# Optimization experiments

Hardware: AMD Instinct MI355X
Metric: run time of the kernel (lower is better)

Reference implementation:

```python
import jax, jax.numpy as jnp
import numpy as np

K = 64            # number of keypoints
PATCH = 16        # patch size
NUM_CLASSES = 1000
K_HARRIS = 0.04


def _conv3x3(x, w):
    # x: [N, Cin, H, W], w: [Cout, Cin, 3, 3], stride 1, padding 1 (torch conv2d = cross-correlation)
    return jax.lax.conv_general_dilated(x, w, (1, 1), 'SAME',
                                        dimension_numbers=('NCHW', 'OIHW', 'NCHW'))


def _harris_coords(x, k, patch_size):
    B, C, H, W = x.shape
    g = jnp.mean(x, axis=1, keepdims=True) if C != 1 else x  # grayscale [B,1,H,W]
    dxk = jnp.array([[-1., 0., 1.], [-1., 0., 1.], [-1., 0., 1.]], x.dtype).reshape(1, 1, 3, 3)
    dyk = jnp.array([[-1., -1., -1.], [0., 0., 0.], [1., 1., 1.]], x.dtype).reshape(1, 1, 3, 3)
    gauss = (jnp.array([[1., 2., 1.], [2., 4., 2.], [1., 2., 1.]], x.dtype) / 16.0).reshape(1, 1, 3, 3)
    dx = _conv3x3(g, dxk)
    dy = _conv3x3(g, dyk)
    Sxx = _conv3x3(dx * dx, gauss)
    Syy = _conv3x3(dy * dy, gauss)
    Sxy = _conv3x3(dx * dy, gauss)
    R = Sxx * Syy - Sxy ** 2 - K_HARRIS * (Sxx + Syy) ** 2  # [B,1,H,W]
    m = patch_size
    mask = jnp.zeros((H, W), x.dtype).at[m:H - m, m:W - m].set(1.0)
    R_flat = (R[:, 0] * mask).reshape(B, -1)
    _, idx = jax.lax.top_k(R_flat, k)                        # [B,k]
    coords = jnp.stack([idx // W, idx % W], axis=-1).astype(jnp.float32)  # (row, col)
    coords = (coords / jnp.array([H, W], jnp.float32) - 0.5) * 2.0
    return jnp.clip(coords, -1.0, 1.0)                       # [B,k,2]


def _grid_sample_bilinear(img, grid):
    # img: [N,C,H,W]; grid: [N,Hg,Wg,2] with (x, y) in [-1,1]; align_corners=True, zeros padding
    N, C, H, W = img.shape
    Hg, Wg = grid.shape[1], grid.shape[2]
    gx = (grid[..., 0] + 1.0) * 0.5 * (W - 1)
    gy = (grid[..., 1] + 1.0) * 0.5 * (H - 1)
    x0 = jnp.floor(gx); y0 = jnp.floor(gy)
    x1 = x0 + 1.0;      y1 = y0 + 1.0
    wx1 = gx - x0; wx0 = 1.0 - wx1
    wy1 = gy - y0; wy0 = 1.0 - wy1

    img_flat = img.reshape(N, C, H * W)

    def gather(xi, yi):
        valid = ((xi >= 0) & (xi < W) & (yi >= 0) & (yi < H)).astype(img.dtype)
        xc = jnp.clip(xi, 0, W - 1).astype(jnp.int32)
        yc = jnp.clip(yi, 0, H - 1).astype(jnp.int32)
        flat = (yc * W + xc).reshape(N, 1, Hg * Wg)
        vals = jnp.take_along_axis(img_flat, flat, axis=2).reshape(N, C, Hg, Wg)
        return vals * valid[:, None]

    out = (gather(x0, y0) * (wx0 * wy0)[:, None]
           + gather(x1, y0) * (wx1 * wy0)[:, None]
           + gather(x0, y1) * (wx0 * wy1)[:, None]
           + gather(x1, y1) * (wx1 * wy1)[:, None])
    return out


def _extract_patches(images, keypoints, patch_size):
    B, C, H, W = images.shape
    k = keypoints.shape[1]
    coords01 = (keypoints + 1.0) / 2.0                       # [B,k,2] (y,x) in [0,1]
    r = patch_size / H
    pg = jnp.linspace(-r, r, patch_size)
    yy, xx = jnp.meshgrid(pg, pg, indexing='ij')
    base = jnp.stack([xx, yy], axis=-1)[None, None]          # [1,1,P,P,2] (x_off, y_off)
    grid = base + coords01[:, :, None, None, :]              # faithful to original broadcast
    grid = grid * 2.0 - 1.0
    grid = grid.reshape(B * k, patch_size, patch_size, 2)
    x_exp = jnp.repeat(images, k, axis=0)                    # repeat_interleave on batch
    patches = _grid_sample_bilinear(x_exp, grid)             # [B*k,C,P,P]
    return patches.reshape(B, k, C, patch_size, patch_size)


def _classify(patches, conv_w, conv_b, fc1_w, fc1_b, fc2_w, fc2_b):
    B, k, C, H, W = patches.shape
    p = patches.reshape(B * k, C, H, W)
    h = _conv3x3(p, conv_w) + conv_b[None, :, None, None]
    h = jax.nn.relu(h)
    h = h.reshape(B * k, -1)                                 # [B*k, 8*P*P]
    h = jax.nn.relu(h @ fc1_w.T + fc1_b)                     # [B*k, 64]
    h = h.reshape(B, k * 64)
    return h @ fc2_w.T + fc2_b                               # [B, num_classes]


def setup_inputs() -> dict:
    key = jax.random.key(0)
    ks = jax.random.split(key, 7)
    B, C, H, W = 32, 3, 224, 224
    return {
        'x': jax.random.normal(ks[0], (B, C, H, W), dtype=jnp.float32),
        'conv_w': jax.random.normal(ks[1], (8, C, 3, 3), dtype=jnp.float32) * 0.1,
        'conv_b': jax.random.normal(ks[2], (8,), dtype=jnp.float32) * 0.05,
        'fc1_w': jax.random.normal(ks[3], (64, 8 * PATCH * PATCH), dtype=jnp.float32) * 0.02,
        'fc1_b': jax.random.normal(ks[4], (64,), dtype=jnp.float32) * 0.05,
        'fc2_w': jax.random.normal(ks[5], (NUM_CLASSES, 64 * K), dtype=jnp.float32) * 0.02,
        'fc2_b': jax.random.normal(ks[6], (NUM_CLASSES,), dtype=jnp.float32) * 0.05,
    }


def reference(x, conv_w, conv_b, fc1_w, fc1_b, fc2_w, fc2_b):
    coords = _harris_coords(x, K, PATCH)                     # [B,K,2]
    patches = _extract_patches(x, coords, PATCH)             # [B,K,C,P,P]
    return _classify(patches, conv_w, conv_b, fc1_w, fc1_b, fc2_w, fc2_b)
```

## Files before the change

### kernel.cpp

```cpp
#include <hip/hip_runtime.h>
#include <cstdint>
#include <math.h>

#define HW 224
#define NPIX (HW*HW)
#define BATCH 32
#define KP 64
#define PS 16
#define NCLS 1000
#define TKW 112
#define FC1_KS 16

__device__ __forceinline__ uint64_t tk_pack(float v, int idx) {
    uint32_t u = __float_as_uint(v);
    u = (u & 0x80000000u) ? ~u : (u | 0x80000000u);
    return ((uint64_t)u << 32) | (uint32_t)(~idx);
}

__device__ __forceinline__ uint64_t tk_sort_asc(uint64_t k, int lane) {
    #pragma unroll
    for (int size = 2; size <= 64; size <<= 1) {
        #pragma unroll
        for (int stride = size >> 1; stride >= 1; stride >>= 1) {
            uint64_t o = __shfl_xor(k, stride, 64);
            bool up = ((lane & size) == 0);
            bool keepmax = (((lane & stride) != 0) == up);
            k = keepmax ? (k > o ? k : o) : (k < o ? k : o);
        }
    }
    return k;
}

__device__ __forceinline__ uint64_t tk_clean_desc(uint64_t k, int lane) {
    #pragma unroll
    for (int stride = 32; stride >= 1; stride >>= 1) {
        uint64_t o = __shfl_xor(k, stride, 64);
        bool keepmax = ((lane & stride) == 0);
        k = keepmax ? (k > o ? k : o) : (k < o ? k : o);
    }
    return k;
}

__global__ __launch_bounds__(256) void k_harris_topk(const float* __restrict__ x,
                                                     uint64_t* __restrict__ cand) {
    const int r = blockIdx.x, b = blockIdx.y;
    const int tid = threadIdx.x;
    const int row0 = r * 8;
    __shared__ float G[12][228];
    __shared__ float DXs[10][228];
    __shared__ float DYs[10][228];
    __shared__ float RB[1792];
    const float* xb = x + (size_t)b * 3 * NPIX;

    for (int l = tid; l < 12 * 224; l += 256) {
        int gr = l / 224, gc = l % 224;
        int gy = row0 - 2 + gr;
        float v = 0.f;
        if (gy >= 0 && gy < HW) {
            int o = gy * HW + gc;
            v = (xb[o] + xb[NPIX + o] + xb[2 * NPIX + o]) / 3.0f;
        }
        G[gr][gc + 1] = v;
    }
    if (tid < 12) { G[tid][0] = 0.f; G[tid][225] = 0.f; }
    if (tid < 10) { DXs[tid][0] = 0.f; DXs[tid][225] = 0.f;
                    DYs[tid][0] = 0.f; DYs[tid][225] = 0.f; }
    __syncthreads();

    for (int rid = tid; rid < 320; rid += 256) {
        int dr = rid >> 5, cb = (rid & 31) * 7;
        int ay = row0 - 1 + dr;
        float g0[9], g1[9], g2[9];
        #pragma unroll
        for (int v = 0; v < 9; v++) {
            g0[v] = G[dr][cb + v];
            g1[v] = G[dr + 1][cb + v];
            g2[v] = G[dr + 2][cb + v];
        }
        bool ok = (ay >= 0 && ay < HW);
        #pragma unroll
        for (int t = 0; t < 7; t++) {
            float dxv = 0.f, dyv = 0.f;
            if (ok) {
                dxv = (g0[t + 2] - g0[t]) + (g1[t + 2] - g1[t]) +
                      (g2[t + 2] - g2[t]);
                dyv = (g2[t] + g2[t + 1] + g2[t + 2]) -
                      (g0[t] + g0[t + 1] + g0[t + 2]);
            }
            DXs[dr][cb + t + 1] = dxv;
            DYs[dr][cb + t + 1] = dyv;
        }
    }
    __syncthreads();

    {
        const int rr = tid >> 5, cb = (tid & 31) * 7;
        const int gy = row0 + rr;
        float dxw[3][9], dyw[3][9];
        #pragma unroll
        for (int u = 0; u < 3; u++)
            #pragma unroll
            for (int v = 0; v < 9; v++) {
                dxw[u][v] = DXs[rr + u][cb + v];
                dyw[u][v] = DYs[rr + u][cb + v];
            }
        const bool rowok = (gy >= PS && gy < HW - PS);
        const float gw[3][3] = {{1.f/16.f, 2.f/16.f, 1.f/16.f},
                                {2.f/16.f, 4.f/16.f, 2.f/16.f},
                                {1.f/16.f, 2.f/16.f, 1.f/16.f}};
        #pragma unroll
        for (int t = 0; t < 7; t++) {
            int c = cb + t;
            float outv = 0.f;
            if (rowok && c >= PS && c < HW - PS) {
                float sxx = 0.f, syy = 0.f, sxy = 0.f;
                #pragma unroll
                for (int u = 0; u < 3; u++)
                    #pragma unroll
                    for (int v = 0; v < 3; v++) {
                        float dv = dxw[u][t + v];
                        float ev = dyw[u][t + v];
                        float w = gw[u][v];
                        sxx += w * dv * dv;
                        syy += w * ev * ev;
                        sxy += w * dv * ev;
                    }
                float tr = sxx + syy;
                outv = sxx * syy - sxy * sxy - 0.04f * tr * tr;
            }
            RB[rr * 224 + c] = outv;
        }
    }
    __syncthreads();

    const int w = tid >> 6, lane = tid & 63;
    const int chunk = w * 448;
    const int gbase = row0 * 224 + chunk;
    uint64_t T = 0;
    #pragma unroll 1
    for (int it = 0; it < 7; it++) {
        float v = RB[chunk + it * 64 + lane];
        uint64_t ck = tk_pack(v, gbase + it * 64 + lane);
        uint64_t thr = __shfl(T, 63, 64);
        if (__ballot(ck > thr)) {
            uint64_t s = tk_sort_asc(ck, lane);
            uint64_t m = (T > s) ? T : s;
            T = tk_clean_desc(m, lane);
        }
    }
    cand[((size_t)b * TKW + r * 4 + w) * 64 + lane] = T;
}

__global__ __launch_bounds__(1024) void k_topk_merge(const uint64_t* __restrict__ cand,
                                                     int* __restrict__ kp) {
    const int img = blockIdx.x;
    const int w = threadIdx.x >> 6, lane = threadIdx.x & 63;
    const uint64_t* cb = cand + (size_t)img * TKW * 64;
    __shared__ uint64_t S[16 * 64];

    uint64_t T = cb[(w * 7) * 64 + lane];
    #pragma unroll
    for (int r = 1; r < 7; r++) {
        uint64_t C = cb[(w * 7 + r) * 64 + (63 - lane)];
        uint64_t m = (T > C) ? T : C;
        T = tk_clean_desc(m, lane);
    }
    S[w * 64 + lane] = T;
    __syncthreads();
    if (w == 0) {
        uint64_t T2 = S[lane];
        #pragma unroll
        for (int r = 1; r < 16; r++) {
            uint64_t C = S[r * 64 + (63 - lane)];
            uint64_t m = (T2 > C) ? T2 : C;
            T2 = tk_clean_desc(m, lane);
        }
        kp[img * KP + lane] = (int)(~(uint32_t)T2);
    }
}

__device__ __forceinline__ float gat4(const float* img, float xf, float yf) {
    bool valid = (xf >= 0.f) && (xf < 224.f) && (yf >= 0.f) && (yf < 224.f);
    if (!valid) return 0.f;
    int xi = (int)fminf(fmaxf(xf, 0.f), 223.f);
    int yi = (int)fminf(fmaxf(yf, 0.f), 223.f);
    return img[yi * HW + xi];
}

__global__ __launch_bounds__(256) void k_patch_conv(
    const float* __restrict__ x, const int* __restrict__ kp,
    const float* __restrict__ conv_w, const float* __restrict__ conv_b,
    float* __restrict__ h) {
    const int s = blockIdx.x;
    const int b = blockIdx.y;
    const int tid = threadIdx.x;

    __shared__ float P[3][18][18];

    const int idx = kp[b * KP + s];
    const int row = idx / HW, col = idx % HW;
    float cy = ((float)row / 224.0f - 0.5f) * 2.0f;
    float cx = ((float)col / 224.0f - 0.5f) * 2.0f;
    cy = fminf(fmaxf(cy, -1.0f), 1.0f);
    cx = fminf(fmaxf(cx, -1.0f), 1.0f);
    const float y01 = (cy + 1.0f) * 0.5f;
    const float x01 = (cx + 1.0f) * 0.5f;
    const float rr = 16.0f / 224.0f;
    const float step = (2.0f * rr) / 15.0f;
    const float* xb = x + (size_t)b * 3 * NPIX;

    for (int e = tid; e < 972; e += 256) {
        int c = e / 324, rem = e - c * 324;
        int yy = rem / 18, xx = rem - yy * 18;
        float val = 0.f;
        if (yy >= 1 && yy <= 16 && xx >= 1 && xx <= 16) {
            int i = yy - 1, j = xx - 1;
            float pj = (j == 15) ? rr : (-rr + (float)j * step);
            float pi = (i == 15) ? rr : (-rr + (float)i * step);
            float gxn = (pj + y01) * 2.0f - 1.0f;
            float gyn = (pi + x01) * 2.0f - 1.0f;
            float gx = (gxn + 1.0f) * 0.5f * 223.0f;
            float gy = (gyn + 1.0f) * 0.5f * 223.0f;
            float x0 = floorf(gx), y0 = floorf(gy);
            float x1 = x0 + 1.0f, y1 = y0 + 1.0f;
            float wx1 = gx - x0, wy1 = gy - y0;
            float wx0 = 1.0f - wx1, wy0 = 1.0f - wy1;
            const float* img = xb + (size_t)c * NPIX;
            val = gat4(img, x0, y0) * (wx0 * wy0)
                + gat4(img, x1, y0) * (wx1 * wy0)
                + gat4(img, x0, y1) * (wx0 * wy1)
                + gat4(img, x1, y1) * (wx1 * wy1);
        }
        P[c][yy][xx] = val;
    }
    __syncthreads();

    const int i = tid >> 4, j = tid & 15;
    float acc[8];
    #pragma unroll
    for (int co = 0; co < 8; co++) acc[co] = conv_b[co];
    #pragma unroll
    for (int ci = 0; ci < 3; ci++) {
        float n[9];
        #pragma unroll
        for (int di = 0; di < 3; di++)
            #pragma unroll
            for (int dj = 0; dj < 3; dj++)
                n[di * 3 + dj] = P[ci][i + di][j + dj];
        #pragma unroll
        for (int co = 0; co < 8; co++) {
            float a = acc[co];
            #pragma unroll
            for (int u = 0; u < 9; u++)
                a += n[u] * conv_w[co * 27 + ci * 9 + u];
            acc[co] = a;
        }
    }
    const size_t mbase = ((size_t)(b * KP + s)) * 2048;
    #pragma unroll
    for (int co = 0; co < 8; co++)
        h[mbase + co * 256 + tid] = fmaxf(acc[co], 0.0f);
}

__global__ __launch_bounds__(256) void k_fc1(
    const float* __restrict__ h, const float* __restrict__ fc1_w,
    float* __restrict__ partial) {
    const int mt = blockIdx.x;
    const int ks = blockIdx.y;
    const int tid = threadIdx.x;
    const int M0 = mt * 64;
    const int og = tid >> 4, mg = tid & 15;
    __shared__ float A[64 * 68];
    __shared__ float W[64 * 68];
    float acc[4][4];
    #pragma unroll
    for (int i = 0; i < 4; i++)
        #pragma unroll
        for (int j = 0; j < 4; j++) acc[i][j] = 0.f;

    #pragma unroll 1
    for (int ch = 0; ch < 2; ch++) {
        const int k0 = ks * 128 + ch * 64;
        __syncthreads();
        #pragma unroll
        for (int p = 0; p < 4; p++) {
            int row = p * 16 + (tid >> 4);
            int c0 = (tid & 15) * 4;
            float4 av = *(const float4*)&h[(size_t)(M0 + row) * 2048 + k0 + c0];
            A[(c0 + 0) * 68 + row] = av.x;
            A[(c0 + 1) * 68 + row] = av.y;
            A[(c0 + 2) * 68 + row] = av.z;
            A[(c0 + 3) * 68 + row] = av.w;
            float4 wv = *(const float4*)&fc1_w[(size_t)row * 2048 + k0 + c0];
            W[(c0 + 0) * 68 + row] = wv.x;
            W[(c0 + 1) * 68 + row] = wv.y;
            W[(c0 + 2) * 68 + row] = wv.z;
            W[(c0 + 3) * 68 + row] = wv.w;
        }
        __syncthreads();
        #pragma unroll 4
        for (int k = 0; k < 64; k++) {
            float4 a = *(float4*)&A[k * 68 + mg * 4];
            float4 w = *(float4*)&W[k * 68 + og * 4];
            acc[0][0] += a.x * w.x; acc[0][1] += a.x * w.y;
            acc[0][2] += a.x * w.z; acc[0][3] += a.x * w.w;
            acc[1][0] += a.y * w.x; acc[1][1] += a.y * w.y;
            acc[1][2] += a.y * w.z; acc[1][3] += a.y * w.w;
            acc[2][0] += a.z * w.x; acc[2][1] += a.z * w.y;
            acc[2][2] += a.z * w.z; acc[2][3] += a.z * w.w;
            acc[3][0] += a.w * w.x; acc[3][1] += a.w * w.y;
            acc[3][2] += a.w * w.z; acc[3][3] += a.w * w.w;
        }
    }
    float* pb = partial + ((size_t)ks * 2048 + M0) * 64;
    #pragma unroll
    for (int mi = 0; mi < 4; mi++) {
        float4 v = make_float4(acc[mi][0], acc[mi][1], acc[mi][2], acc[mi][3]);
        *(float4*)&pb[(mg * 4 + mi) * 64 + og * 4] = v;
    }
}

__global__ __launch_bounds__(256) void k_fc1_post(
    const float* __restrict__ partial, const float* __restrict__ fc1_b,
    const float* __restrict__ fc2_b, float* __restrict__ feat,
    float* __restrict__ out) {
    const int id = blockIdx.x * 256 + threadIdx.x;
    const int o = id & 63;
    float s = 0.f;
    #pragma unroll
    for (int ks = 0; ks < FC1_KS; ks++) s += partial[(size_t)ks * 131072 + id];
    s = fmaxf(s + fc1_b[o], 0.f);
    feat[id] = s;
    if (id < BATCH * NCLS) out[id] = fc2_b[id % NCLS];
}

__global__ __launch_bounds__(256) void k_fc2(
    const float* __restrict__ feat, const float* __restrict__ fc2_w,
    float* __restrict__ out) {
    const int c0 = blockIdx.x * 8;
    const int kbase = blockIdx.y * 256;
    const int tid = threadIdx.x;
    const int bq = tid & 7, kg = tid >> 3;

    __shared__ float U[8192];
    float* F2 = U;
    float* Wc = U + 32 * 132;
    float* Red = U;

    float4 acc[8];
    #pragma unroll
    for (int cl = 0; cl < 8; cl++) acc[cl] = make_float4(0.f, 0.f, 0.f, 0.f);

    #pragma unroll 1
    for (int ch = 0; ch < 2; ch++) {
        const int k0 = kbase + ch * 128;
        __syncthreads();
        #pragma unroll
        for (int it = 0; it < 4; it++) {
            int l = it * 256 + tid;
            int bb = l >> 5, kc = (l & 31) << 2;
            *(float4*)&F2[bb * 132 + kc] =
                *(const float4*)&feat[(size_t)bb * 4096 + k0 + kc];
        }
        {
            int cl = tid >> 5, kc = (tid & 31) << 2;
            *(float4*)&Wc[cl * 128 + kc] =
                *(const float4*)&fc2_w[(size_t)(c0 + cl) * 4096 + k0 + kc];
        }
        __syncthreads();
        float4 f0 = *(float4*)&F2[(bq * 4 + 0) * 132 + kg * 4];
        float4 f1 = *(float4*)&F2[(bq * 4 + 1) * 132 + kg * 4];
        float4 f2 = *(float4*)&F2[(bq * 4 + 2) * 132 + kg * 4];
        float4 f3 = *(float4*)&F2[(bq * 4 + 3) * 132 + kg * 4];
        #pragma unroll
        for (int cl = 0; cl < 8; cl++) {
            float4 w = *(float4*)&Wc[cl * 128 + kg * 4];
            acc[cl].x += w.x * f0.x + w.y * f0.y + w.z * f0.z + w.w * f0.w;
            acc[cl].y += w.x * f1.x + w.y * f1.y + w.z * f1.z + w.w * f1.w;
            acc[cl].z += w.x * f2.x + w.y * f2.y + w.z * f2.z + w.w * f2.w;
            acc[cl].w += w.x * f3.x + w.y * f3.y + w.z * f3.z + w.w * f3.w;
        }
    }

    __syncthreads();
    #pragma unroll
    for (int cl = 0; cl < 8; cl++)
        *(float4*)&Red[kg * 256 + cl * 32 + bq * 4] = acc[cl];
    __syncthreads();

    const int cl2 = tid >> 5, b2 = tid & 31;
    float s = 0.f;
    #pragma unroll
    for (int g = 0; g < 32; g++) s += Red[g * 256 + cl2 * 32 + b2];
    atomicAdd(&out[b2 * NCLS + c0 + cl2], s);
}

extern "C" void kernel_launch(void* const* d_in, const int* in_sizes, int n_in,
                              void* d_out, int out_size, void* d_ws, size_t ws_size,
                              hipStream_t stream) {
    const float* x      = (const float*)d_in[0];
    const float* conv_w = (const float*)d_in[1];
    const float* conv_b = (const float*)d_in[2];
    const float* fc1_w  = (const float*)d_in[3];
    const float* fc1_b  = (const float*)d_in[4];
    const float* fc2_w  = (const float*)d_in[5];
    const float* fc2_b  = (const float*)d_in[6];
    float* out = (float*)d_out;

    char* base = (char*)d_ws;
    const size_t region0 = (size_t)FC1_KS * 2048 * 64 * 4;
    uint64_t* cand    = (uint64_t*)base;
    float*    partial = (float*)base;
    float*    h       = (float*)(base + region0);
    float*    feat    = h + (size_t)2048 * 2048;
    int*      kp      = (int*)(feat + (size_t)4096 * 32);

    k_harris_topk<<<dim3(28, 32), 256, 0, stream>>>(x, cand);
    k_topk_merge<<<32, 1024, 0, stream>>>(cand, kp);
    k_patch_conv<<<dim3(KP, BATCH), 256, 0, stream>>>(x, kp, conv_w, conv_b, h);
    k_fc1<<<dim3(32, FC1_KS), 256, 0, stream>>>(h, fc1_w, partial);
    k_fc1_post<<<512, 256, 0, stream>>>(partial, fc1_b, fc2_b, feat, out);
    k_fc2<<<dim3(125, 16), 256, 0, stream>>>(feat, fc2_w, out);
}
```

Baseline: 169.9 us.

## Use DPP/swizzle shuffles in bitonic top-k and merge wave candidates in-block

Replaces the generic __shfl_xor calls in the bitonic sort and clean stages with DPP moves and ds_swizzle for small strides, avoiding LDS-routed permutes. Each Harris block now merges its four per-wave top-64 lists in shared memory before writing, so it emits 28 candidate lists per image instead of 112. The merge kernel shrinks to 256 threads with a two-level merge over the 28 lists. The aim is less shuffle latency and less candidate traffic and merge work, at the cost of extra syncs and serial merge steps in the Harris kernel.

```diff
diff --git a/kernel.cpp b/kernel.cpp
--- a/kernel.cpp
+++ b/kernel.cpp
@@ -8,7 +8,7 @@
 #define KP 64
 #define PS 16
 #define NCLS 1000
-#define TKW 112
+#define TKB 28
 #define FC1_KS 16
 
 __device__ __forceinline__ uint64_t tk_pack(float v, int idx) {
@@ -17,27 +17,46 @@
     return ((uint64_t)u << 32) | (uint32_t)(~idx);
 }
 
+template<int S>
+__device__ __forceinline__ uint64_t sx64(uint64_t k) {
+    uint32_t lo = (uint32_t)k, hi = (uint32_t)(k >> 32);
+    if constexpr (S == 1) {
+        lo = (uint32_t)__builtin_amdgcn_mov_dpp((int)lo, 0xB1, 0xF, 0xF, true);
+        hi = (uint32_t)__builtin_amdgcn_mov_dpp((int)hi, 0xB1, 0xF, 0xF, true);
+    } else if constexpr (S == 2) {
+        lo = (uint32_t)__builtin_amdgcn_mov_dpp((int)lo, 0x4E, 0xF, 0xF, true);
+        hi = (uint32_t)__builtin_amdgcn_mov_dpp((int)hi, 0x4E, 0xF, 0xF, true);
+    } else if constexpr (S <= 16) {
+        constexpr int imm = (S << 10) | 0x1F;
+        lo = (uint32_t)__builtin_amdgcn_ds_swizzle((int)lo, imm);
+        hi = (uint32_t)__builtin_amdgcn_ds_swizzle((int)hi, imm);
+    } else {
+        lo = (uint32_t)__shfl_xor((int)lo, 32, 64);
+        hi = (uint32_t)__shfl_xor((int)hi, 32, 64);
+    }
+    return ((uint64_t)hi << 32) | lo;
+}
+
+#define BSTAGE(SIZE, S) { uint64_t o = sx64<S>(k); \
+    bool keepmax = (((lane & S) != 0) == ((lane & SIZE) == 0)); \
+    k = keepmax ? (k > o ? k : o) : (k < o ? k : o); }
+
 __device__ __forceinline__ uint64_t tk_sort_asc(uint64_t k, int lane) {
-    #pragma unroll
-    for (int size = 2; size <= 64; size <<= 1) {
-        #pragma unroll
-        for (int stride = size >> 1; stride >= 1; stride >>= 1) {
-            uint64_t o = __shfl_xor(k, stride, 64);
-            bool up = ((lane & size) == 0);
-            bool keepmax = (((lane & stride) != 0) == up);
-            k = keepmax ? (k > o ? k : o) : (k < o ? k : o);
-        }
-    }
+    BSTAGE(2,1)
+    BSTAGE(4,2)  BSTAGE(4,1)
+    BSTAGE(8,4)  BSTAGE(8,2)  BSTAGE(8,1)
+    BSTAGE(16,8) BSTAGE(16,4) BSTAGE(16,2) BSTAGE(16,1)
+    BSTAGE(32,16) BSTAGE(32,8) BSTAGE(32,4) BSTAGE(32,2) BSTAGE(32,1)
+    BSTAGE(64,32) BSTAGE(64,16) BSTAGE(64,8) BSTAGE(64,4) BSTAGE(64,2) BSTAGE(64,1)
     return k;
 }
 
+#define CSTAGE(S) { uint64_t o = sx64<S>(k); \
+    bool keepmax = ((lane & S) == 0); \
+    k = keepmax ? (k > o ? k : o) : (k < o ? k : o); }
+
 __device__ __forceinline__ uint64_t tk_clean_desc(uint64_t k, int lane) {
-    #pragma unroll
-    for (int stride = 32; stride >= 1; stride >>= 1) {
-        uint64_t o = __shfl_xor(k, stride, 64);
-        bool keepmax = ((lane & stride) == 0);
-        k = keepmax ? (k > o ? k : o) : (k < o ? k : o);
-    }
+    CSTAGE(32) CSTAGE(16) CSTAGE(8) CSTAGE(4) CSTAGE(2) CSTAGE(1)
     return k;
 }
 
@@ -50,6 +69,7 @@
     __shared__ float DXs[10][228];
     __shared__ float DYs[10][228];
     __shared__ float RB[1792];
+    __shared__ uint64_t SM[4][64];
     const float* xb = x + (size_t)b * 3 * NPIX;
 
     for (int l = tid; l < 12 * 224; l += 256) {
@@ -148,15 +168,30 @@
             T = tk_clean_desc(m, lane);
         }
     }
-    cand[((size_t)b * TKW + r * 4 + w) * 64 + lane] = T;
-}
-
-__global__ __launch_bounds__(1024) void k_topk_merge(const uint64_t* __restrict__ cand,
-                                                     int* __restrict__ kp) {
+
+    SM[w][lane] = T;
+    __syncthreads();
+    if (w == 0 || w == 2) {
+        uint64_t C = SM[w + 1][63 - lane];
+        uint64_t m = (T > C) ? T : C;
+        T = tk_clean_desc(m, lane);
+        SM[w][lane] = T;
+    }
+    __syncthreads();
+    if (w == 0) {
+        uint64_t C = SM[2][63 - lane];
+        uint64_t m = (T > C) ? T : C;
+        T = tk_clean_desc(m, lane);
+        cand[((size_t)b * TKB + r) * 64 + lane] = T;
+    }
+}
+
+__global__ __launch_bounds__(256) void k_topk_merge(const uint64_t* __restrict__ cand,
+                                                    int* __restrict__ kp) {
     const int img = blockIdx.x;
     const int w = threadIdx.x >> 6, lane = threadIdx.x & 63;
-    const uint64_t* cb = cand + (size_t)img * TKW * 64;
-    __shared__ uint64_t S[16 * 64];
+    const uint64_t* cb = cand + (size_t)img * TKB * 64;
+    __shared__ uint64_t S[4][64];
 
     uint64_t T = cb[(w * 7) * 64 + lane];
     #pragma unroll
@@ -165,17 +200,16 @@
         uint64_t m = (T > C) ? T : C;
         T = tk_clean_desc(m, lane);
     }
-    S[w * 64 + lane] = T;
+    S[w][lane] = T;
     __syncthreads();
     if (w == 0) {
-        uint64_t T2 = S[lane];
-        #pragma unroll
-        for (int r = 1; r < 16; r++) {
-            uint64_t C = S[r * 64 + (63 - lane)];
-            uint64_t m = (T2 > C) ? T2 : C;
-            T2 = tk_clean_desc(m, lane);
-        }
-        kp[img * KP + lane] = (int)(~(uint32_t)T2);
+        #pragma unroll
+        for (int r = 1; r < 4; r++) {
+            uint64_t C = S[r][63 - lane];
+            uint64_t m = (T > C) ? T : C;
+            T = tk_clean_desc(m, lane);
+        }
+        kp[img * KP + lane] = (int)(~(uint32_t)T);
     }
 }
 
@@ -416,7 +450,7 @@
     int*      kp      = (int*)(feat + (size_t)4096 * 32);
 
     k_harris_topk<<<dim3(28, 32), 256, 0, stream>>>(x, cand);
-    k_topk_merge<<<32, 1024, 0, stream>>>(cand, kp);
+    k_topk_merge<<<32, 256, 0, stream>>>(cand, kp);
     k_patch_conv<<<dim3(KP, BATCH), 256, 0, stream>>>(x, kp, conv_w, conv_b, h);
     k_fc1<<<dim3(32, FC1_KS), 256, 0, stream>>>(h, fc1_w, partial);
     k_fc1_post<<<512, 256, 0, stream>>>(partial, fc1_b, fc2_b, feat, out);
```

Measured after the change: 161.2 us, median of 2. 5.2% less time.
